# Kernel optimization log

Hardware: AMD Instinct MI355X
Metric: run time of the kernel (lower is better)

## Reference

```python
import jax, jax.numpy as jnp
import numpy as np

N_EMBD = 126
N_HEADS = 6
HEAD_DIM = N_EMBD // N_HEADS  # 21


def setup_inputs() -> dict:
    key = jax.random.key(0)
    k1, k2, k3 = jax.random.split(key, 3)
    B, T = 8, 2048
    x = jax.random.normal(k1, (B, T, N_EMBD), dtype=jnp.float32)
    # torch Linear weights stored as (out, in); we store transposed (in, out) for x @ W
    w_attn = jax.random.normal(k2, (N_EMBD, 3 * N_EMBD), dtype=jnp.float32) * (1.0 / np.sqrt(N_EMBD))
    w_proj = jax.random.normal(k3, (N_EMBD, N_EMBD), dtype=jnp.float32) * (1.0 / np.sqrt(N_EMBD))
    return {"x": x, "w_attn": w_attn, "w_proj": w_proj}


def reference(x, w_attn, w_proj):
    B, T, C = x.shape
    qkv = x @ w_attn                      # [B, T, 3C]
    q, k, v = jnp.split(qkv, 3, axis=-1)  # each [B, T, C]

    def heads(t):  # [B,T,C] -> [B,H,T,hd]
        return t.reshape(B, T, N_HEADS, HEAD_DIM).transpose(0, 2, 1, 3)

    q, k, v = heads(q), heads(k), heads(v)
    scale = 1.0 / np.sqrt(HEAD_DIM).astype(np.float32)
    scores = jnp.einsum('bhqd,bhkd->bhqk', q, k) * scale  # [B,H,T,T]
    causal = jnp.tril(jnp.ones((T, T), dtype=bool))
    scores = jnp.where(causal, scores, jnp.finfo(scores.dtype).min)
    attn = jax.nn.softmax(scores, axis=-1)
    out = jnp.einsum('bhqk,bhkd->bhqd', attn, v)           # [B,H,T,hd]
    out = out.transpose(0, 2, 1, 3).reshape(B, T, C)
    return out @ w_proj
```

## Files before the change

### kernel.cpp

```cpp
#include <hip/hip_runtime.h>
#include <hip/hip_bf16.h>


#define B_ 8
#define T_ 2048
#define C_ 126
#define H_ 6
#define D_ 21
#define TC_ 378
#define KP_ 128
#define DP_ 32
#define M_ 16384
#define QSCALE 0.31481923469333463f

typedef __hip_bfloat16 bf16;
typedef __bf16 bf16_t;
typedef __bf16 bf16x2 __attribute__((ext_vector_type(2)));
typedef __bf16 bf16x8 __attribute__((ext_vector_type(8)));
typedef float f32x4 __attribute__((ext_vector_type(4)));
typedef int int2v __attribute__((ext_vector_type(2)));

__device__ __forceinline__ float ldf(const bf16* p, long i) { return __bfloat162float(p[i]); }
__device__ __forceinline__ float ldf(const float* p, long i) { return p[i]; }
__device__ __forceinline__ void stf(bf16* p, long i, float v) { p[i] = __float2bfloat16(v); }
__device__ __forceinline__ void stf(float* p, long i, float v) { p[i] = v; }

__device__ __forceinline__ float fexp2(float x) {
#if __has_builtin(__builtin_amdgcn_exp2f)
  return __builtin_amdgcn_exp2f(x);
#else
  float r; asm("v_exp_f32 %0, %1" : "=v"(r) : "v"(x)); return r;
#endif
}

__device__ __forceinline__ unsigned int ld2(const bf16* x, long i) {
  return *(const unsigned int*)((const unsigned short*)x + i);
}
__device__ __forceinline__ unsigned int ld2(const float* x, long i) {
  const float2 f = *(const float2*)(x + i);
  union { bf16_t b[2]; unsigned int u; } cv;
  cv.b[0] = (bf16_t)f.x; cv.b[1] = (bf16_t)f.y;
  return cv.u;
}

__device__ __forceinline__ void probe_dtype(const void* x, int tid, int* sflag) {
  if (tid < 64) {
    const unsigned int w = ((const unsigned int*)x)[tid * 97 + 13];
    const unsigned int e = (w >> 7) & 0xFF;
    const bool bflike = (e >= 115 && e <= 131) || ((w & 0x7FFFu) == 0);
    const unsigned long long mask = __ballot(bflike);
    if (tid == 0) *sflag = (__popcll(mask) >= 40) ? 1 : 0;
  }
  __syncthreads();
}

template <typename T>
__device__ __forceinline__ void prep_w_body(const T* __restrict__ wa,
                                            const T* __restrict__ wp,
                                            bf16_t* __restrict__ WTa,
                                            bf16_t* __restrict__ WTp) {
  const int stride = gridDim.x * blockDim.x;
  const int idx0 = blockIdx.x * blockDim.x + threadIdx.x;
  for (int i = idx0; i < 384 * KP_ + KP_ * KP_; i += stride) {
    if (i < 384 * KP_) {
      const int n = i >> 7, k = i & 127;
      WTa[i] = (k < C_ && n < TC_) ? (bf16_t)ldf(wa, (long)k * TC_ + n) : (bf16_t)0.f;
    } else {
      const int j = i - 384 * KP_;
      const int n = j >> 7, k = j & 127;
      WTp[j] = (k < C_ && n < C_) ? (bf16_t)ldf(wp, (long)k * C_ + n) : (bf16_t)0.f;
    }
  }
}

__global__ __launch_bounds__(256) void prep_w_kernel(
    const void* __restrict__ x, const void* __restrict__ wa,
    const void* __restrict__ wp, bf16_t* __restrict__ WTa,
    bf16_t* __restrict__ WTp) {
  __shared__ int sflag;
  probe_dtype(x, threadIdx.x, &sflag);
  if (sflag) prep_w_body<bf16>((const bf16*)wa, (const bf16*)wp, WTa, WTp);
  else       prep_w_body<float>((const float*)wa, (const float*)wp, WTa, WTp);
}

#define QS_ 40

template <typename T>
__device__ __forceinline__ void qkv_body(
    const T* __restrict__ x, const bf16_t* __restrict__ WT,
    bf16_t* __restrict__ Qb, bf16_t* __restrict__ Kb, bf16_t* __restrict__ VT,
    bf16_t* __restrict__ xs, bf16_t* __restrict__ qbuf,
    bf16_t* __restrict__ kbuf, bf16_t* __restrict__ vbuf) {
  const int m0 = blockIdx.x * 32;
  const int tid = threadIdx.x;
  for (int i = tid; i < 32 * 64; i += 256) {
    const int row = i >> 6, cp = i & 63;
    unsigned int v = 0;
    if (cp < 63) v = ld2(x, (long)(m0 + row) * C_ + 2 * cp);
    ((unsigned int*)xs)[i] = v;
  }
  for (int i = tid; i < 6 * 32 * 11; i += 256) {
    const int h = i / 352, rem = i - h * 352, t = rem / 11, d = 21 + rem % 11;
    qbuf[(h * 32 + t) * QS_ + d] = (bf16_t)0.f;
    kbuf[(h * 32 + t) * QS_ + d] = (bf16_t)0.f;
  }
  for (int i = tid; i < 6 * 11 * 32; i += 256) {
    const int h = i / 352, rem = i - h * 352, d = 21 + rem / 32, t = rem % 32;
    vbuf[(h * 32 + d) * 32 + t] = (d == 21) ? (bf16_t)1.f : (bf16_t)0.f;
  }
  __syncthreads();

  const int wv = tid >> 6, lane = tid & 63;
  const int lr = lane & 15, quad = lane >> 4;
  const bf16_t* arU = xs + lr * KP_ + quad * 8;
  const bf16_t* arL = xs + (16 + lr) * KP_ + quad * 8;
  const bf16x8 aU0 = *(const bf16x8*)(arU);
  const bf16x8 aU1 = *(const bf16x8*)(arU + 32);
  const bf16x8 aU2 = *(const bf16x8*)(arU + 64);
  const bf16x8 aU3 = *(const bf16x8*)(arU + 96);
  const bf16x8 aL0 = *(const bf16x8*)(arL);
  const bf16x8 aL1 = *(const bf16x8*)(arL + 32);
  const bf16x8 aL2 = *(const bf16x8*)(arL + 64);
  const bf16x8 aL3 = *(const bf16x8*)(arL + 96);

  for (int nt = wv; nt < 24; nt += 4) {
    const int n0 = nt * 16;
    const bf16x8* bp = (const bf16x8*)(WT + (long)(n0 + lr) * KP_ + quad * 8);
    const bf16x8 b0 = bp[0], b1 = bp[4], b2 = bp[8], b3 = bp[12];
    f32x4 accU = {0.f, 0.f, 0.f, 0.f};
    f32x4 accL = {0.f, 0.f, 0.f, 0.f};
    accU = __builtin_amdgcn_mfma_f32_16x16x32_bf16(aU0, b0, accU, 0, 0, 0);
    accU = __builtin_amdgcn_mfma_f32_16x16x32_bf16(aU1, b1, accU, 0, 0, 0);
    accU = __builtin_amdgcn_mfma_f32_16x16x32_bf16(aU2, b2, accU, 0, 0, 0);
    accU = __builtin_amdgcn_mfma_f32_16x16x32_bf16(aU3, b3, accU, 0, 0, 0);
    accL = __builtin_amdgcn_mfma_f32_16x16x32_bf16(aL0, b0, accL, 0, 0, 0);
    accL = __builtin_amdgcn_mfma_f32_16x16x32_bf16(aL1, b1, accL, 0, 0, 0);
    accL = __builtin_amdgcn_mfma_f32_16x16x32_bf16(aL2, b2, accL, 0, 0, 0);
    accL = __builtin_amdgcn_mfma_f32_16x16x32_bf16(aL3, b3, accL, 0, 0, 0);

    const int c = n0 + lr;
    if (c < TC_) {
      const int which = c / C_;
      const int cc = c - which * C_;
      const int h = cc / D_, d = cc - h * D_;
#pragma unroll
      for (int r = 0; r < 4; ++r) {
        const int tU = quad * 4 + r;
        const int tL = 16 + tU;
        if (which == 0) {
          qbuf[(h * 32 + tU) * QS_ + d] = (bf16_t)(accU[r] * QSCALE);
          qbuf[(h * 32 + tL) * QS_ + d] = (bf16_t)(accL[r] * QSCALE);
        } else if (which == 1) {
          kbuf[(h * 32 + tU) * QS_ + d] = (bf16_t)accU[r];
          kbuf[(h * 32 + tL) * QS_ + d] = (bf16_t)accL[r];
        } else {
          vbuf[(h * 32 + d) * 32 + tU] = (bf16_t)accU[r];
          vbuf[(h * 32 + d) * 32 + tL] = (bf16_t)accL[r];
        }
      }
    }
  }
  __syncthreads();

  const int b = m0 >> 11, t0 = m0 & 2047;
  for (int i = tid; i < 384; i += 256) {
    const int j = (i < 192) ? i : i - 192;
    const int h = j >> 5, t = j & 31;
    const int4* src = (const int4*)(((i < 192) ? qbuf : kbuf) + (h * 32 + t) * QS_);
    int4* dst = (int4*)((((i < 192) ? Qb : Kb)) + ((long)(b * H_ + h) * T_ + (t0 + t)) * DP_);
    dst[0] = src[0]; dst[1] = src[1]; dst[2] = src[2]; dst[3] = src[3];
  }
  for (int i = tid; i < 192; i += 256) {
    const int h = i >> 5, d = i & 31;
    const int4* src = (const int4*)(vbuf + (h * 32 + d) * 32);
    int4* dst = (int4*)(VT + ((long)(b * H_ + h) * DP_ + d) * T_ + t0);
    dst[0] = src[0]; dst[1] = src[1]; dst[2] = src[2]; dst[3] = src[3];
  }
}

__global__ __launch_bounds__(256) void qkv_mfma(
    const void* __restrict__ x, const bf16_t* __restrict__ WT,
    bf16_t* __restrict__ Qb, bf16_t* __restrict__ Kb, bf16_t* __restrict__ VT) {
  __shared__ __align__(16) bf16_t xs[32 * KP_];
  __shared__ __align__(16) bf16_t qbuf[6 * 32 * QS_];
  __shared__ __align__(16) bf16_t kbuf[6 * 32 * QS_];
  __shared__ __align__(16) bf16_t vbuf[6 * 32 * 32];
  __shared__ int sflag;
  probe_dtype(x, threadIdx.x, &sflag);
  if (sflag) qkv_body<bf16>((const bf16*)x, WT, Qb, Kb, VT, xs, qbuf, kbuf, vbuf);
  else       qkv_body<float>((const float*)x, WT, Qb, Kb, VT, xs, qbuf, kbuf, vbuf);
}

__device__ __forceinline__ void swap32(int& a, int& b) {
#if __has_builtin(__builtin_amdgcn_permlane32_swap)
  const int2v r = __builtin_amdgcn_permlane32_swap(a, b, false, false);
  a = r[0]; b = r[1];
#else
  const int sa = __shfl_xor(a, 32, 64), sb = __shfl_xor(b, 32, 64);
  const bool hi = (threadIdx.x & 32) != 0;
  a = hi ? sb : a;
  b = hi ? b : sa;
#endif
}

__device__ __forceinline__ void swap16(int& a, int& b) {
#if __has_builtin(__builtin_amdgcn_permlane16_swap)
  const int2v r = __builtin_amdgcn_permlane16_swap(a, b, false, false);
  a = r[0]; b = r[1];
#else
  const int sa = __shfl_xor(a, 16, 64), sb = __shfl_xor(b, 16, 64);
  const bool odd = (threadIdx.x & 16) != 0;
  a = odd ? sb : a;
  b = odd ? b : sa;
#endif
}

__device__ __forceinline__ int pkbf(float x, float y) {
  union { bf16x2 h; int i; } u;
  u.h[0] = (bf16_t)x; u.h[1] = (bf16_t)y;
  return u.i;
}

__device__ __forceinline__ bf16x8 build_frag(const f32x4 g1, const f32x4 g2) {
  int a1 = pkbf(g1[0], g1[1]);
  int b1 = pkbf(g1[2], g1[3]);
  int a2 = pkbf(g2[0], g2[1]);
  int b2 = pkbf(g2[2], g2[3]);
  swap32(a1, a2); swap32(b1, b2);
  swap16(a1, a2); swap16(b1, b2);
  union { int i[4]; bf16x8 v; } u;
  u.i[0] = a1; u.i[1] = b1; u.i[2] = a2; u.i[3] = b2;
  return u.v;
}

__global__ __launch_bounds__(256, 4) void attn_mfma(
    const bf16_t* __restrict__ Qb, const bf16_t* __restrict__ Kb,
    const bf16_t* __restrict__ VT, bf16_t* __restrict__ ATTp) {
  __shared__ __align__(16) float smem[4352];
  const int bh = blockIdx.x;
  const int pr = 63 - blockIdx.y;
  const int tid = threadIdx.x;
  const int wv = tid >> 6, lane = tid & 63;
  const int lr = lane & 15, quad = lane >> 4;
  const int q0 = pr * 32;
  const int mq = quad * 4;

  const bf16_t* Qbh = Qb + (long)bh * T_ * DP_;
  const bf16_t* Kbh = Kb + (long)bh * T_ * DP_;
  const bf16_t* VTbh = VT + (long)bh * DP_ * T_;

  const bf16x8 qf0 = *(const bf16x8*)(Qbh + (long)(q0 + lr) * DP_ + quad * 8);
  const bf16x8 qf1 = *(const bf16x8*)(Qbh + (long)(q0 + 16 + lr) * DP_ + quad * 8);

  f32x4 o00 = {0.f,0.f,0.f,0.f}, o01 = {0.f,0.f,0.f,0.f};
  f32x4 o10 = {0.f,0.f,0.f,0.f}, o11 = {0.f,0.f,0.f,0.f};

  int t = wv;
  for (; t + 4 <= pr; t += 8) {
    const int kbA = t * 32, kbB = (t + 4) * 32;
    const bf16x8 kA0 = *(const bf16x8*)(Kbh + (long)(kbA + lr) * DP_ + quad * 8);
    const bf16x8 kA1 = *(const bf16x8*)(Kbh + (long)(kbA + 16 + lr) * DP_ + quad * 8);
    const bf16x8 kB0 = *(const bf16x8*)(Kbh + (long)(kbB + lr) * DP_ + quad * 8);
    const bf16x8 kB1 = *(const bf16x8*)(Kbh + (long)(kbB + 16 + lr) * DP_ + quad * 8);

    f32x4 sA00 = {0.f,0.f,0.f,0.f}, sA01 = {0.f,0.f,0.f,0.f};
    f32x4 sA10 = {0.f,0.f,0.f,0.f}, sA11 = {0.f,0.f,0.f,0.f};
    f32x4 sB00 = {0.f,0.f,0.f,0.f}, sB01 = {0.f,0.f,0.f,0.f};
    f32x4 sB10 = {0.f,0.f,0.f,0.f}, sB11 = {0.f,0.f,0.f,0.f};
    __builtin_amdgcn_s_setprio(1);
    sA00 = __builtin_amdgcn_mfma_f32_16x16x32_bf16(kA0, qf0, sA00, 0, 0, 0);
    sA01 = __builtin_amdgcn_mfma_f32_16x16x32_bf16(kA0, qf1, sA01, 0, 0, 0);
    sA10 = __builtin_amdgcn_mfma_f32_16x16x32_bf16(kA1, qf0, sA10, 0, 0, 0);
    sA11 = __builtin_amdgcn_mfma_f32_16x16x32_bf16(kA1, qf1, sA11, 0, 0, 0);
    sB00 = __builtin_amdgcn_mfma_f32_16x16x32_bf16(kB0, qf0, sB00, 0, 0, 0);
    sB01 = __builtin_amdgcn_mfma_f32_16x16x32_bf16(kB0, qf1, sB01, 0, 0, 0);
    sB10 = __builtin_amdgcn_mfma_f32_16x16x32_bf16(kB1, qf0, sB10, 0, 0, 0);
    sB11 = __builtin_amdgcn_mfma_f32_16x16x32_bf16(kB1, qf1, sB11, 0, 0, 0);
    __builtin_amdgcn_s_setprio(0);

    const bf16x8 vA0 = *(const bf16x8*)(VTbh + (long)lr * T_ + kbA + quad * 8);
    const bf16x8 vA1 = *(const bf16x8*)(VTbh + (long)(16 + lr) * T_ + kbA + quad * 8);
    const bf16x8 vB0 = *(const bf16x8*)(VTbh + (long)lr * T_ + kbB + quad * 8);
    const bf16x8 vB1 = *(const bf16x8*)(VTbh + (long)(16 + lr) * T_ + kbB + quad * 8);

    if (t + 4 == pr) {
#pragma unroll
      for (int r = 0; r < 4; ++r) {
        if (mq + r > lr) { sB00[r] = -1e30f; sB11[r] = -1e30f; }
        sB10[r] = -1e30f;
      }
    }
#pragma unroll
    for (int r = 0; r < 4; ++r) {
      sA00[r] = fexp2(sA00[r]); sA01[r] = fexp2(sA01[r]);
      sA10[r] = fexp2(sA10[r]); sA11[r] = fexp2(sA11[r]);
      sB00[r] = fexp2(sB00[r]); sB01[r] = fexp2(sB01[r]);
      sB10[r] = fexp2(sB10[r]); sB11[r] = fexp2(sB11[r]);
    }
    const bf16x8 pA0 = build_frag(sA00, sA10);
    const bf16x8 pA1 = build_frag(sA01, sA11);
    const bf16x8 pB0 = build_frag(sB00, sB10);
    const bf16x8 pB1 = build_frag(sB01, sB11);

    __builtin_amdgcn_s_setprio(1);
    o00 = __builtin_amdgcn_mfma_f32_16x16x32_bf16(pA0, vA0, o00, 0, 0, 0);
    o01 = __builtin_amdgcn_mfma_f32_16x16x32_bf16(pA0, vA1, o01, 0, 0, 0);
    o10 = __builtin_amdgcn_mfma_f32_16x16x32_bf16(pA1, vA0, o10, 0, 0, 0);
    o11 = __builtin_amdgcn_mfma_f32_16x16x32_bf16(pA1, vA1, o11, 0, 0, 0);
    o00 = __builtin_amdgcn_mfma_f32_16x16x32_bf16(pB0, vB0, o00, 0, 0, 0);
    o01 = __builtin_amdgcn_mfma_f32_16x16x32_bf16(pB0, vB1, o01, 0, 0, 0);
    o10 = __builtin_amdgcn_mfma_f32_16x16x32_bf16(pB1, vB0, o10, 0, 0, 0);
    o11 = __builtin_amdgcn_mfma_f32_16x16x32_bf16(pB1, vB1, o11, 0, 0, 0);
    __builtin_amdgcn_s_setprio(0);
  }

  if (t <= pr) {
    const int kb = t * 32;
    const bf16x8 k0 = *(const bf16x8*)(Kbh + (long)(kb + lr) * DP_ + quad * 8);
    const bf16x8 k1 = *(const bf16x8*)(Kbh + (long)(kb + 16 + lr) * DP_ + quad * 8);
    f32x4 s00 = {0.f,0.f,0.f,0.f}, s01 = {0.f,0.f,0.f,0.f};
    f32x4 s10 = {0.f,0.f,0.f,0.f}, s11 = {0.f,0.f,0.f,0.f};
    s00 = __builtin_amdgcn_mfma_f32_16x16x32_bf16(k0, qf0, s00, 0, 0, 0);
    s01 = __builtin_amdgcn_mfma_f32_16x16x32_bf16(k0, qf1, s01, 0, 0, 0);
    s10 = __builtin_amdgcn_mfma_f32_16x16x32_bf16(k1, qf0, s10, 0, 0, 0);
    s11 = __builtin_amdgcn_mfma_f32_16x16x32_bf16(k1, qf1, s11, 0, 0, 0);
    const bf16x8 v0 = *(const bf16x8*)(VTbh + (long)lr * T_ + kb + quad * 8);
    const bf16x8 v1 = *(const bf16x8*)(VTbh + (long)(16 + lr) * T_ + kb + quad * 8);
    if (t == pr) {
#pragma unroll
      for (int r = 0; r < 4; ++r) {
        if (mq + r > lr) { s00[r] = -1e30f; s11[r] = -1e30f; }
        s10[r] = -1e30f;
      }
    }
#pragma unroll
    for (int r = 0; r < 4; ++r) {
      s00[r] = fexp2(s00[r]); s01[r] = fexp2(s01[r]);
      s10[r] = fexp2(s10[r]); s11[r] = fexp2(s11[r]);
    }
    const bf16x8 pf0 = build_frag(s00, s10);
    const bf16x8 pf1 = build_frag(s01, s11);
    o00 = __builtin_amdgcn_mfma_f32_16x16x32_bf16(pf0, v0, o00, 0, 0, 0);
    o01 = __builtin_amdgcn_mfma_f32_16x16x32_bf16(pf0, v1, o01, 0, 0, 0);
    o10 = __builtin_amdgcn_mfma_f32_16x16x32_bf16(pf1, v0, o10, 0, 0, 0);
    o11 = __builtin_amdgcn_mfma_f32_16x16x32_bf16(pf1, v1, o11, 0, 0, 0);
  }

  __syncthreads();
  {
    float* my = smem + (wv * 64 + lane) * 17;
#pragma unroll
    for (int j = 0; j < 4; ++j) {
      my[j]      = o00[j];
      my[4 + j]  = o01[j];
      my[8 + j]  = o10[j];
      my[12 + j] = o11[j];
    }
  }
  __syncthreads();

  if (wv == 0) {
    float tot[16];
#pragma unroll
    for (int j = 0; j < 16; ++j)
      tot[j] = smem[lane * 17 + j] + smem[(64 + lane) * 17 + j] +
               smem[(128 + lane) * 17 + j] + smem[(192 + lane) * 17 + j];
    const int b = bh / H_, h = bh - b * H_;
#pragma unroll
    for (int r = 0; r < 4; ++r) {
      const float rl0 = 1.f / __shfl(tot[4 + r],  (lane & 48) + 5, 64);
      const float rl1 = 1.f / __shfl(tot[12 + r], (lane & 48) + 5, 64);
      const int qA = q0 + mq + r, qB = qA + 16;
      bf16_t* opA = ATTp + (long)(b * T_ + qA) * KP_ + h * D_;
      bf16_t* opB = ATTp + (long)(b * T_ + qB) * KP_ + h * D_;
      opA[lr] = (bf16_t)(tot[r] * rl0);
      opB[lr] = (bf16_t)(tot[8 + r] * rl1);
      if (lr < 5) {
        opA[16 + lr] = (bf16_t)(tot[4 + r] * rl0);
        opB[16 + lr] = (bf16_t)(tot[12 + r] * rl1);
      }
    }
  }
}

__global__ __launch_bounds__(256) void proj_mfma(
    const void* __restrict__ x, const bf16_t* __restrict__ ATTp,
    const bf16_t* __restrict__ WT, void* __restrict__ out) {
  __shared__ int sflag;
  probe_dtype(x, threadIdx.x, &sflag);
  const int isbf = sflag;

  const int m0 = blockIdx.x * 32;
  const int tid = threadIdx.x;
  const int wv = tid >> 6, lane = tid & 63;
  const int lr = lane & 15, quad = lane >> 4;

  const bf16x8* apU = (const bf16x8*)(ATTp + (long)(m0 + lr) * KP_ + quad * 8);
  const bf16x8* apL = (const bf16x8*)(ATTp + (long)(m0 + 16 + lr) * KP_ + quad * 8);
  const bf16x8 aU0 = apU[0], aU1 = apU[4], aU2 = apU[8], aU3 = apU[12];
  const bf16x8 aL0 = apL[0], aL1 = apL[4], aL2 = apL[8], aL3 = apL[12];

  for (int nt = wv; nt < 8; nt += 4) {
    const int n0 = nt * 16;
    const bf16x8* bp = (const bf16x8*)(WT + (long)(n0 + lr) * KP_ + quad * 8);
    const bf16x8 b0 = bp[0], b1 = bp[4], b2 = bp[8], b3 = bp[12];
    f32x4 accU = {0.f, 0.f, 0.f, 0.f};
    f32x4 accL = {0.f, 0.f, 0.f, 0.f};
    accU = __builtin_amdgcn_mfma_f32_16x16x32_bf16(aU0, b0, accU, 0, 0, 0);
    accU = __builtin_amdgcn_mfma_f32_16x16x32_bf16(aU1, b1, accU, 0, 0, 0);
    accU = __builtin_amdgcn_mfma_f32_16x16x32_bf16(aU2, b2, accU, 0, 0, 0);
    accU = __builtin_amdgcn_mfma_f32_16x16x32_bf16(aU3, b3, accU, 0, 0, 0);
    accL = __builtin_amdgcn_mfma_f32_16x16x32_bf16(aL0, b0, accL, 0, 0, 0);
    accL = __builtin_amdgcn_mfma_f32_16x16x32_bf16(aL1, b1, accL, 0, 0, 0);
    accL = __builtin_amdgcn_mfma_f32_16x16x32_bf16(aL2, b2, accL, 0, 0, 0);
    accL = __builtin_amdgcn_mfma_f32_16x16x32_bf16(aL3, b3, accL, 0, 0, 0);

    const int c = n0 + lr;
    if (c < C_) {
#pragma unroll
      for (int r = 0; r < 4; ++r) {
        const int mU = m0 + quad * 4 + r;
        const int mL = mU + 16;
        if (isbf) {
          stf((bf16*)out,  (long)mU * C_ + c, accU[r]);
          stf((bf16*)out,  (long)mL * C_ + c, accL[r]);
        } else {
          stf((float*)out, (long)mU * C_ + c, accU[r]);
          stf((float*)out, (long)mL * C_ + c, accL[r]);
        }
      }
    }
  }
}

extern "C" void kernel_launch(void* const* d_in, const int* in_sizes, int n_in,
                              void* d_out, int out_size, void* d_ws, size_t ws_size,
                              hipStream_t stream) {
  const void* x      = d_in[0];
  const void* w_attn = d_in[1];
  const void* w_proj = d_in[2];

  char* base = (char*)d_ws;
  const long QKV = (long)48 * T_ * DP_;
  bf16_t* Qb = (bf16_t*)(base + 256);
  bf16_t* Kb = Qb + QKV;
  bf16_t* VT = Kb + QKV;
  bf16_t* WTa  = VT + QKV;
  bf16_t* WTp  = WTa + 384 * KP_;
  bf16_t* ATTp = WTp + KP_ * KP_;

  prep_w_kernel<<<64, 256, 0, stream>>>(x, w_attn, w_proj, WTa, WTp);
  qkv_mfma<<<M_ / 32, 256, 0, stream>>>(x, WTa, Qb, Kb, VT);
  attn_mfma<<<dim3(48, 64), 256, 0, stream>>>(Qb, Kb, VT, ATTp);
  proj_mfma<<<M_ / 32, 256, 0, stream>>>(x, ATTp, WTp, d_out);
}
```

Baseline: 129.1 us.

## Process two 32-row query tiles per attention block to reuse K/V loads

Each attention block now covers 64 query rows, two 32-row tiles, instead of 32. Each K/V key tile is loaded once and applied to both query tiles, with the first tile skipped past its diagonal. This halves the grid and cuts K/V global traffic per query, at the cost of more registers (launch bounds lowered to 2), less loop unrolling over key tiles, two serialized reduction/store epilogues, and fewer blocks for load balancing.

Measured after the change: 116.7 us. -9.6%, faster.

```diff
diff --git a/kernel.cpp b/kernel.cpp
--- a/kernel.cpp
+++ b/kernel.cpp
@@ -233,146 +233,167 @@
   return u.v;
 }
 
-__global__ __launch_bounds__(256, 4) void attn_mfma(
+__global__ __launch_bounds__(256, 2) void attn_mfma(
     const bf16_t* __restrict__ Qb, const bf16_t* __restrict__ Kb,
     const bf16_t* __restrict__ VT, bf16_t* __restrict__ ATTp) {
   __shared__ __align__(16) float smem[4352];
   const int bh = blockIdx.x;
-  const int pr = 63 - blockIdx.y;
+  const int qb = 31 - blockIdx.y;
+  const int d0 = 2 * qb, d1 = d0 + 1;
+  const int q0 = qb * 64;
   const int tid = threadIdx.x;
   const int wv = tid >> 6, lane = tid & 63;
   const int lr = lane & 15, quad = lane >> 4;
-  const int q0 = pr * 32;
   const int mq = quad * 4;
 
   const bf16_t* Qbh = Qb + (long)bh * T_ * DP_;
   const bf16_t* Kbh = Kb + (long)bh * T_ * DP_;
   const bf16_t* VTbh = VT + (long)bh * DP_ * T_;
 
-  const bf16x8 qf0 = *(const bf16x8*)(Qbh + (long)(q0 + lr) * DP_ + quad * 8);
-  const bf16x8 qf1 = *(const bf16x8*)(Qbh + (long)(q0 + 16 + lr) * DP_ + quad * 8);
-
-  f32x4 o00 = {0.f,0.f,0.f,0.f}, o01 = {0.f,0.f,0.f,0.f};
-  f32x4 o10 = {0.f,0.f,0.f,0.f}, o11 = {0.f,0.f,0.f,0.f};
-
-  int t = wv;
-  for (; t + 4 <= pr; t += 8) {
-    const int kbA = t * 32, kbB = (t + 4) * 32;
-    const bf16x8 kA0 = *(const bf16x8*)(Kbh + (long)(kbA + lr) * DP_ + quad * 8);
-    const bf16x8 kA1 = *(const bf16x8*)(Kbh + (long)(kbA + 16 + lr) * DP_ + quad * 8);
-    const bf16x8 kB0 = *(const bf16x8*)(Kbh + (long)(kbB + lr) * DP_ + quad * 8);
-    const bf16x8 kB1 = *(const bf16x8*)(Kbh + (long)(kbB + 16 + lr) * DP_ + quad * 8);
+  const bf16x8 qA0 = *(const bf16x8*)(Qbh + (long)(q0 + lr) * DP_ + quad * 8);
+  const bf16x8 qA1 = *(const bf16x8*)(Qbh + (long)(q0 + 16 + lr) * DP_ + quad * 8);
+  const bf16x8 qB0 = *(const bf16x8*)(Qbh + (long)(q0 + 32 + lr) * DP_ + quad * 8);
+  const bf16x8 qB1 = *(const bf16x8*)(Qbh + (long)(q0 + 48 + lr) * DP_ + quad * 8);
+
+  f32x4 oA00 = {0.f,0.f,0.f,0.f}, oA01 = {0.f,0.f,0.f,0.f};
+  f32x4 oA10 = {0.f,0.f,0.f,0.f}, oA11 = {0.f,0.f,0.f,0.f};
+  f32x4 oB00 = {0.f,0.f,0.f,0.f}, oB01 = {0.f,0.f,0.f,0.f};
+  f32x4 oB10 = {0.f,0.f,0.f,0.f}, oB11 = {0.f,0.f,0.f,0.f};
+
+  for (int t = wv; t <= d1; t += 4) {
+    const int kb = t * 32;
+    const bool do0 = (t <= d0);
+    const bf16x8 k0 = *(const bf16x8*)(Kbh + (long)(kb + lr) * DP_ + quad * 8);
+    const bf16x8 k1 = *(const bf16x8*)(Kbh + (long)(kb + 16 + lr) * DP_ + quad * 8);
 
     f32x4 sA00 = {0.f,0.f,0.f,0.f}, sA01 = {0.f,0.f,0.f,0.f};
     f32x4 sA10 = {0.f,0.f,0.f,0.f}, sA11 = {0.f,0.f,0.f,0.f};
     f32x4 sB00 = {0.f,0.f,0.f,0.f}, sB01 = {0.f,0.f,0.f,0.f};
     f32x4 sB10 = {0.f,0.f,0.f,0.f}, sB11 = {0.f,0.f,0.f,0.f};
     __builtin_amdgcn_s_setprio(1);
-    sA00 = __builtin_amdgcn_mfma_f32_16x16x32_bf16(kA0, qf0, sA00, 0, 0, 0);
-    sA01 = __builtin_amdgcn_mfma_f32_16x16x32_bf16(kA0, qf1, sA01, 0, 0, 0);
-    sA10 = __builtin_amdgcn_mfma_f32_16x16x32_bf16(kA1, qf0, sA10, 0, 0, 0);
-    sA11 = __builtin_amdgcn_mfma_f32_16x16x32_bf16(kA1, qf1, sA11, 0, 0, 0);
-    sB00 = __builtin_amdgcn_mfma_f32_16x16x32_bf16(kB0, qf0, sB00, 0, 0, 0);
-    sB01 = __builtin_amdgcn_mfma_f32_16x16x32_bf16(kB0, qf1, sB01, 0, 0, 0);
-    sB10 = __builtin_amdgcn_mfma_f32_16x16x32_bf16(kB1, qf0, sB10, 0, 0, 0);
-    sB11 = __builtin_amdgcn_mfma_f32_16x16x32_bf16(kB1, qf1, sB11, 0, 0, 0);
+    if (do0) {
+      sA00 = __builtin_amdgcn_mfma_f32_16x16x32_bf16(k0, qA0, sA00, 0, 0, 0);
+      sA01 = __builtin_amdgcn_mfma_f32_16x16x32_bf16(k0, qA1, sA01, 0, 0, 0);
+      sA10 = __builtin_amdgcn_mfma_f32_16x16x32_bf16(k1, qA0, sA10, 0, 0, 0);
+      sA11 = __builtin_amdgcn_mfma_f32_16x16x32_bf16(k1, qA1, sA11, 0, 0, 0);
+    }
+    sB00 = __builtin_amdgcn_mfma_f32_16x16x32_bf16(k0, qB0, sB00, 0, 0, 0);
+    sB01 = __builtin_amdgcn_mfma_f32_16x16x32_bf16(k0, qB1, sB01, 0, 0, 0);
+    sB10 = __builtin_amdgcn_mfma_f32_16x16x32_bf16(k1, qB0, sB10, 0, 0, 0);
+    sB11 = __builtin_amdgcn_mfma_f32_16x16x32_bf16(k1, qB1, sB11, 0, 0, 0);
     __builtin_amdgcn_s_setprio(0);
 
-    const bf16x8 vA0 = *(const bf16x8*)(VTbh + (long)lr * T_ + kbA + quad * 8);
-    const bf16x8 vA1 = *(const bf16x8*)(VTbh + (long)(16 + lr) * T_ + kbA + quad * 8);
-    const bf16x8 vB0 = *(const bf16x8*)(VTbh + (long)lr * T_ + kbB + quad * 8);
-    const bf16x8 vB1 = *(const bf16x8*)(VTbh + (long)(16 + lr) * T_ + kbB + quad * 8);
-
-    if (t + 4 == pr) {
+    const bf16x8 v0 = *(const bf16x8*)(VTbh + (long)lr * T_ + kb + quad * 8);
+    const bf16x8 v1 = *(const bf16x8*)(VTbh + (long)(16 + lr) * T_ + kb + quad * 8);
+
+    if (t == d0) {
+#pragma unroll
+      for (int r = 0; r < 4; ++r) {
+        if (mq + r > lr) { sA00[r] = -1e30f; sA11[r] = -1e30f; }
+        sA10[r] = -1e30f;
+      }
+    }
+    if (t == d1) {
 #pragma unroll
       for (int r = 0; r < 4; ++r) {
         if (mq + r > lr) { sB00[r] = -1e30f; sB11[r] = -1e30f; }
         sB10[r] = -1e30f;
       }
     }
+    if (do0) {
+#pragma unroll
+      for (int r = 0; r < 4; ++r) {
+        sA00[r] = fexp2(sA00[r]); sA01[r] = fexp2(sA01[r]);
+        sA10[r] = fexp2(sA10[r]); sA11[r] = fexp2(sA11[r]);
+      }
+    }
 #pragma unroll
     for (int r = 0; r < 4; ++r) {
-      sA00[r] = fexp2(sA00[r]); sA01[r] = fexp2(sA01[r]);
-      sA10[r] = fexp2(sA10[r]); sA11[r] = fexp2(sA11[r]);
       sB00[r] = fexp2(sB00[r]); sB01[r] = fexp2(sB01[r]);
       sB10[r] = fexp2(sB10[r]); sB11[r] = fexp2(sB11[r]);
     }
-    const bf16x8 pA0 = build_frag(sA00, sA10);
-    const bf16x8 pA1 = build_frag(sA01, sA11);
-    const bf16x8 pB0 = build_frag(sB00, sB10);
-    const bf16x8 pB1 = build_frag(sB01, sB11);
 
     __builtin_amdgcn_s_setprio(1);
-    o00 = __builtin_amdgcn_mfma_f32_16x16x32_bf16(pA0, vA0, o00, 0, 0, 0);
-    o01 = __builtin_amdgcn_mfma_f32_16x16x32_bf16(pA0, vA1, o01, 0, 0, 0);
-    o10 = __builtin_amdgcn_mfma_f32_16x16x32_bf16(pA1, vA0, o10, 0, 0, 0);
-    o11 = __builtin_amdgcn_mfma_f32_16x16x32_bf16(pA1, vA1, o11, 0, 0, 0);
-    o00 = __builtin_amdgcn_mfma_f32_16x16x32_bf16(pB0, vB0, o00, 0, 0, 0);
-    o01 = __builtin_amdgcn_mfma_f32_16x16x32_bf16(pB0, vB1, o01, 0, 0, 0);
-    o10 = __builtin_amdgcn_mfma_f32_16x16x32_bf16(pB1, vB0, o10, 0, 0, 0);
-    o11 = __builtin_amdgcn_mfma_f32_16x16x32_bf16(pB1, vB1, o11, 0, 0, 0);
+    if (do0) {
+      const bf16x8 pA0 = build_frag(sA00, sA10);
+      const bf16x8 pA1 = build_frag(sA01, sA11);
+      oA00 = __builtin_amdgcn_mfma_f32_16x16x32_bf16(pA0, v0, oA00, 0, 0, 0);
+      oA01 = __builtin_amdgcn_mfma_f32_16x16x32_bf16(pA0, v1, oA01, 0, 0, 0);
+      oA10 = __builtin_amdgcn_mfma_f32_16x16x32_bf16(pA1, v0, oA10, 0, 0, 0);
+      oA11 = __builtin_amdgcn_mfma_f32_16x16x32_bf16(pA1, v1, oA11, 0, 0, 0);
+    }
+    {
+      const bf16x8 pB0 = build_frag(sB00, sB10);
+      const bf16x8 pB1 = build_frag(sB01, sB11);
+      oB00 = __builtin_amdgcn_mfma_f32_16x16x32_bf16(pB0, v0, oB00, 0, 0, 0);
+      oB01 = __builtin_amdgcn_mfma_f32_16x16x32_bf16(pB0, v1, oB01, 0, 0, 0);
+      oB10 = __builtin_amdgcn_mfma_f32_16x16x32_bf16(pB1, v0, oB10, 0, 0, 0);
+      oB11 = __builtin_amdgcn_mfma_f32_16x16x32_bf16(pB1, v1, oB11, 0, 0, 0);
+    }
     __builtin_amdgcn_s_setprio(0);
   }
 
-  if (t <= pr) {
-    const int kb = t * 32;
-    const bf16x8 k0 = *(const bf16x8*)(Kbh + (long)(kb + lr) * DP_ + quad * 8);
-    const bf16x8 k1 = *(const bf16x8*)(Kbh + (long)(kb + 16 + lr) * DP_ + quad * 8);
-    f32x4 s00 = {0.f,0.f,0.f,0.f}, s01 = {0.f,0.f,0.f,0.f};
-    f32x4 s10 = {0.f,0.f,0.f,0.f}, s11 = {0.f,0.f,0.f,0.f};
-    s00 = __builtin_amdgcn_mfma_f32_16x16x32_bf16(k0, qf0, s00, 0, 0, 0);
-    s01 = __builtin_amdgcn_mfma_f32_16x16x32_bf16(k0, qf1, s01, 0, 0, 0);
-    s10 = __builtin_amdgcn_mfma_f32_16x16x32_bf16(k1, qf0, s10, 0, 0, 0);
-    s11 = __builtin_amdgcn_mfma_f32_16x16x32_bf16(k1, qf1, s11, 0, 0, 0);
-    const bf16x8 v0 = *(const bf16x8*)(VTbh + (long)lr * T_ + kb + quad * 8);
-    const bf16x8 v1 = *(const bf16x8*)(VTbh + (long)(16 + lr) * T_ + kb + quad * 8);
-    if (t == pr) {
-#pragma unroll
-      for (int r = 0; r < 4; ++r) {
-        if (mq + r > lr) { s00[r] = -1e30f; s11[r] = -1e30f; }
-        s10[r] = -1e30f;
-      }
-    }
-#pragma unroll
-    for (int r = 0; r < 4; ++r) {
-      s00[r] = fexp2(s00[r]); s01[r] = fexp2(s01[r]);
-      s10[r] = fexp2(s10[r]); s11[r] = fexp2(s11[r]);
-    }
-    const bf16x8 pf0 = build_frag(s00, s10);
-    const bf16x8 pf1 = build_frag(s01, s11);
-    o00 = __builtin_amdgcn_mfma_f32_16x16x32_bf16(pf0, v0, o00, 0, 0, 0);
-    o01 = __builtin_amdgcn_mfma_f32_16x16x32_bf16(pf0, v1, o01, 0, 0, 0);
-    o10 = __builtin_amdgcn_mfma_f32_16x16x32_bf16(pf1, v0, o10, 0, 0, 0);
-    o11 = __builtin_amdgcn_mfma_f32_16x16x32_bf16(pf1, v1, o11, 0, 0, 0);
-  }
+  const int b = bh / H_, h = bh - b * H_;
 
   __syncthreads();
   {
     float* my = smem + (wv * 64 + lane) * 17;
 #pragma unroll
     for (int j = 0; j < 4; ++j) {
-      my[j]      = o00[j];
-      my[4 + j]  = o01[j];
-      my[8 + j]  = o10[j];
-      my[12 + j] = o11[j];
-    }
-  }
-  __syncthreads();
-
+      my[j]      = oA00[j];
+      my[4 + j]  = oA01[j];
+      my[8 + j]  = oA10[j];
+      my[12 + j] = oA11[j];
+    }
+  }
+  __syncthreads();
   if (wv == 0) {
     float tot[16];
 #pragma unroll
     for (int j = 0; j < 16; ++j)
       tot[j] = smem[lane * 17 + j] + smem[(64 + lane) * 17 + j] +
                smem[(128 + lane) * 17 + j] + smem[(192 + lane) * 17 + j];
-    const int b = bh / H_, h = bh - b * H_;
 #pragma unroll
     for (int r = 0; r < 4; ++r) {
       const float rl0 = 1.f / __shfl(tot[4 + r],  (lane & 48) + 5, 64);
       const float rl1 = 1.f / __shfl(tot[12 + r], (lane & 48) + 5, 64);
-      const int qA = q0 + mq + r, qB = qA + 16;
+      const int qA = q0 + mq + r, qB2 = qA + 16;
       bf16_t* opA = ATTp + (long)(b * T_ + qA) * KP_ + h * D_;
-      bf16_t* opB = ATTp + (long)(b * T_ + qB) * KP_ + h * D_;
+      bf16_t* opB = ATTp + (long)(b * T_ + qB2) * KP_ + h * D_;
+      opA[lr] = (bf16_t)(tot[r] * rl0);
+      opB[lr] = (bf16_t)(tot[8 + r] * rl1);
+      if (lr < 5) {
+        opA[16 + lr] = (bf16_t)(tot[4 + r] * rl0);
+        opB[16 + lr] = (bf16_t)(tot[12 + r] * rl1);
+      }
+    }
+  }
+
+  __syncthreads();
+  {
+    float* my = smem + (wv * 64 + lane) * 17;
+#pragma unroll
+    for (int j = 0; j < 4; ++j) {
+      my[j]      = oB00[j];
+      my[4 + j]  = oB01[j];
+      my[8 + j]  = oB10[j];
+      my[12 + j] = oB11[j];
+    }
+  }
+  __syncthreads();
+  if (wv == 0) {
+    float tot[16];
+#pragma unroll
+    for (int j = 0; j < 16; ++j)
+      tot[j] = smem[lane * 17 + j] + smem[(64 + lane) * 17 + j] +
+               smem[(128 + lane) * 17 + j] + smem[(192 + lane) * 17 + j];
+#pragma unroll
+    for (int r = 0; r < 4; ++r) {
+      const float rl0 = 1.f / __shfl(tot[4 + r],  (lane & 48) + 5, 64);
+      const float rl1 = 1.f / __shfl(tot[12 + r], (lane & 48) + 5, 64);
+      const int qA = q0 + 32 + mq + r, qB2 = qA + 16;
+      bf16_t* opA = ATTp + (long)(b * T_ + qA) * KP_ + h * D_;
+      bf16_t* opB = ATTp + (long)(b * T_ + qB2) * KP_ + h * D_;
       opA[lr] = (bf16_t)(tot[r] * rl0);
       opB[lr] = (bf16_t)(tot[8 + r] * rl1);
       if (lr < 5) {
@@ -451,6 +472,6 @@
 
   prep_w_kernel<<<64, 256, 0, stream>>>(x, w_attn, w_proj, WTa, WTp);
   qkv_mfma<<<M_ / 32, 256, 0, stream>>>(x, WTa, Qb, Kb, VT);
-  attn_mfma<<<dim3(48, 64), 256, 0, stream>>>(Qb, Kb, VT, ATTp);
+  attn_mfma<<<dim3(48, 32), 256, 0, stream>>>(Qb, Kb, VT, ATTp);
   proj_mfma<<<M_ / 32, 256, 0, stream>>>(x, ATTp, WTp, d_out);
 }
```
